# Optimization experiments

Hardware: AMD Instinct MI355X
Metric: run time of the kernel (lower is better)

Reference implementation:

```python
import jax, jax.numpy as jnp
import numpy as np

N = 100000
IN_DIM = 128
HID = 128
HEADS = 2
OUT_DIM = 2
E = 800000
NEG_SLOPE = 0.2


def setup_inputs() -> dict:
    key = jax.random.key(0)
    ks = jax.random.split(key, 12)
    x = jax.random.normal(ks[0], (N, IN_DIM), dtype=jnp.float32)
    edge_index = jax.random.randint(ks[1], (2, E), 0, N, dtype=jnp.int64)
    s = 0.05
    # GATConv layer 1: in=128 -> heads=2, out=128
    W1 = jax.random.normal(ks[2], (IN_DIM, HEADS * HID), dtype=jnp.float32) * s
    a_src1 = jax.random.normal(ks[3], (HEADS, HID), dtype=jnp.float32) * s
    a_dst1 = jax.random.normal(ks[4], (HEADS, HID), dtype=jnp.float32) * s
    b1 = jnp.zeros((HEADS * HID,), dtype=jnp.float32)
    # GATConv layer 2: in=256 -> heads=2, out=128
    W2 = jax.random.normal(ks[5], (HEADS * HID, HEADS * HID), dtype=jnp.float32) * s
    a_src2 = jax.random.normal(ks[6], (HEADS, HID), dtype=jnp.float32) * s
    a_dst2 = jax.random.normal(ks[7], (HEADS, HID), dtype=jnp.float32) * s
    b2 = jnp.zeros((HEADS * HID,), dtype=jnp.float32)
    # post_mp: Linear(256,128) -> Dropout(eval, no-op) -> Linear(128,2)
    Wp1 = jax.random.normal(ks[8], (HEADS * HID, HID), dtype=jnp.float32) * s
    bp1 = jnp.zeros((HID,), dtype=jnp.float32)
    Wp2 = jax.random.normal(ks[9], (HID, OUT_DIM), dtype=jnp.float32) * s
    bp2 = jnp.zeros((OUT_DIM,), dtype=jnp.float32)
    return {"x": x, "edge_index": edge_index,
            "W1": W1, "a_src1": a_src1, "a_dst1": a_dst1, "b1": b1,
            "W2": W2, "a_src2": a_src2, "a_dst2": a_dst2, "b2": b2,
            "Wp1": Wp1, "bp1": bp1, "Wp2": Wp2, "bp2": bp2}


def gat_conv(x, src, dst, W, a_src, a_dst, b):
    # linear transform, split heads: [N, H, C]
    h = (x @ W).reshape(-1, HEADS, HID)
    # per-node attention logits: [N, H]
    alpha_src = jnp.sum(h * a_src, axis=-1)
    alpha_dst = jnp.sum(h * a_dst, axis=-1)
    # per-edge logits, edge e = (src -> dst): [E, H]
    e = jax.nn.leaky_relu(alpha_src[src] + alpha_dst[dst], NEG_SLOPE)
    # segment softmax over incoming edges of each destination node
    m = jax.ops.segment_max(e, dst, num_segments=N)
    e = jnp.exp(e - m[dst])
    denom = jax.ops.segment_sum(e, dst, num_segments=N)
    alpha = e / (denom[dst] + 1e-16)
    # gather source features, weight, scatter-add to destinations
    msg = h[src] * alpha[:, :, None]            # [E, H, C]
    out = jax.ops.segment_sum(msg, dst, num_segments=N)  # [N, H, C]
    return out.reshape(-1, HEADS * HID) + b


def reference(x, edge_index, W1, a_src1, a_dst1, b1, W2, a_src2, a_dst2, b2,
              Wp1, bp1, Wp2, bp2):
    # add self-loops (PyG GATConv default)
    loops = jnp.arange(N, dtype=edge_index.dtype)
    src = jnp.concatenate([edge_index[0], loops])
    dst = jnp.concatenate([edge_index[1], loops])
    h = jax.nn.relu(gat_conv(x, src, dst, W1, a_src1, a_dst1, b1))
    h = jax.nn.relu(gat_conv(h, src, dst, W2, a_src2, a_dst2, b2))
    h = h @ Wp1 + bp1          # post_mp Linear 1 (dropout is eval no-op)
    h = h @ Wp2 + bp2          # post_mp Linear 2
    return jax.nn.sigmoid(h)
```

## Files before the change

### kernel.cpp

```cpp
#include <hip/hip_runtime.h>
#include <hip/hip_bf16.h>
#include <math.h>

#define NNODES 100000
#define NPAD   100032
#define IN_DIM 128
#define HID 128
#define HEADS 2
#define F2 256
#define NEDGES 800000
#define ETOT 900000
#define NEG_SLOPE 0.2f
#define MB 1563
#define EDGE_BLOCKS 3516

typedef unsigned int uint;
typedef unsigned short ushort;
typedef __attribute__((ext_vector_type(8))) short short8;
typedef __attribute__((ext_vector_type(4))) float floatx4;

__device__ __forceinline__ ushort f2bf(float f) {
    uint u = __builtin_bit_cast(uint, f);
    u += 0x7fffu + ((u >> 16) & 1u);
    return (ushort)(u >> 16);
}
__device__ __forceinline__ float bf2f(uint u16) {
    return __builtin_bit_cast(float, u16 << 16);
}
__device__ __forceinline__ float wred_sum(float v) {
    for (int o = 32; o; o >>= 1) v += __shfl_xor(v, o);
    return v;
}

__device__ __forceinline__ void gld16(const ushort* g, ushort* l) {
    __builtin_amdgcn_global_load_lds(
        (const __attribute__((address_space(1))) unsigned int*)(uintptr_t)g,
        (__attribute__((address_space(3))) unsigned int*)(unsigned int)(uintptr_t)l,
        16, 0, 0);
}

__global__ __launch_bounds__(256) void scan1_kernel(const int* __restrict__ deg,
                                                    int* __restrict__ row_start,
                                                    int* __restrict__ bsum) {
    __shared__ int s[256];
    int t = threadIdx.x;
    int i = blockIdx.x * 256 + t;
    int v = (i < NNODES) ? deg[i] : 0;
    s[t] = v;
    __syncthreads();
    for (int off = 1; off < 256; off <<= 1) {
        int x = (t >= off) ? s[t - off] : 0;
        __syncthreads();
        s[t] += x;
        __syncthreads();
    }
    if (i < NNODES) row_start[i] = s[t] - v;
    if (t == 255) bsum[blockIdx.x] = s[255];
}

__global__ __launch_bounds__(256) void scan_fix_kernel(int* __restrict__ row_start,
                                                       const int* __restrict__ bsum,
                                                       int* __restrict__ cursor) {
    __shared__ int sh[256];
    int t = threadIdx.x, bid = blockIdx.x;
    int v = 0;
    for (int k = t; k < bid; k += 256) v += bsum[k];
    sh[t] = v;
    __syncthreads();
    for (int off = 128; off; off >>= 1) {
        if (t < off) sh[t] += sh[t + off];
        __syncthreads();
    }
    int boff = sh[0];
    int i = bid * 256 + t;
    if (i == 0) row_start[NNODES] = ETOT;
    if (i < NNODES) {
        int r = row_start[i] + boff;
        row_start[i] = r;
        cursor[i] = r;
    }
}

__global__ __launch_bounds__(256) void prep_hist_kernel(const int* __restrict__ ei,
                                                        int* __restrict__ deg,
                                                        const float* __restrict__ W1,
                                                        ushort* __restrict__ W1t,
                                                        const float* __restrict__ W2,
                                                        ushort* __restrict__ W2t,
                                                        const float* __restrict__ Wp1,
                                                        const float* __restrict__ bp1,
                                                        const float* __restrict__ Wp2,
                                                        const float* __restrict__ bp2,
                                                        float2* __restrict__ Wf,
                                                        float* __restrict__ bfv,
                                                        const float* __restrict__ x,
                                                        ushort* __restrict__ xbf) {
    int b = blockIdx.x, t = threadIdx.x;
    if (b < EDGE_BLOCKS) {
        int i = b * 256 + t;
        if (i < ETOT) {
            int dst = (i < NEDGES) ? ei[NEDGES + i] : (i - NEDGES);
            atomicAdd(&deg[dst], 1);
        }
        return;
    }
    int bb = b - EDGE_BLOCKS;
    if (bb < 128) {
        int i = bb * 256 + t;
        int n = i >> 7, k = i & 127;
        W1t[n * 128 + k] = f2bf(W1[k * 256 + n]);
    } else if (bb < 384) {
        int i = (bb - 128) * 256 + t;
        int n = i >> 8, k = i & 255;
        W2t[n * 256 + k] = f2bf(W2[k * 256 + n]);
    } else if (bb == 384) {
        float s0 = 0.f, s1 = 0.f;
        for (int m = 0; m < 128; m++) {
            float w = Wp1[t * 128 + m];
            s0 += w * Wp2[2 * m];
            s1 += w * Wp2[2 * m + 1];
        }
        Wf[t] = make_float2(s0, s1);
        if (t < 2) {
            float bb2 = bp2[t];
            for (int m = 0; m < 128; m++) bb2 += bp1[m] * Wp2[2 * m + t];
            bfv[t] = bb2;
        }
    } else {
        size_t i = (size_t)(bb - 385) * 2048 + t * 8;
        float4 f0 = *reinterpret_cast<const float4*>(&x[i]);
        float4 f1 = *reinterpret_cast<const float4*>(&x[i + 4]);
        uint4 o;
        o.x = (uint)f2bf(f0.x) | ((uint)f2bf(f0.y) << 16);
        o.y = (uint)f2bf(f0.z) | ((uint)f2bf(f0.w) << 16);
        o.z = (uint)f2bf(f1.x) | ((uint)f2bf(f1.y) << 16);
        o.w = (uint)f2bf(f1.z) | ((uint)f2bf(f1.w) << 16);
        *reinterpret_cast<uint4*>(&xbf[i]) = o;
    }
}

__device__ __forceinline__ void gemm_body(int mb, int head,
                                          const ushort* __restrict__ A,
                                          const ushort* __restrict__ Bt,
                                          ushort* __restrict__ C,
                                          float* __restrict__ as_f,
                                          float* __restrict__ ad_f,
                                          const float* __restrict__ aS,
                                          const float* __restrict__ aD,
                                          int K, ushort* smem) {
    int t = threadIdx.x;
    int wave = t >> 6, lane = t & 63;
    int quad = lane >> 4, l16 = lane & 15;
    size_t rowBase = (size_t)mb * 64;
    int colBase = head * 128;

    floatx4 acc[8];
#pragma unroll
    for (int i = 0; i < 8; i++) acc[i] = (floatx4){0.f, 0.f, 0.f, 0.f};

    int srow = lane >> 2;
    int scg  = (lane & 3) ^ ((lane >> 3) & 3);
    const ushort* gA  = A  + (rowBase + wave * 16 + srow) * (size_t)K + scg * 8;
    const ushort* gB0 = Bt + (size_t)(colBase + wave * 16 + srow) * K + scg * 8;
    const ushort* gB1 = gB0 + (size_t)64 * K;
    ushort* lA  = smem + wave * 512;
    ushort* lB0 = smem + 2048 + wave * 512;
    ushort* lB1 = lB0 + 2048;

    const char* sb = (const char*)smem;
    int xs = (quad ^ ((l16 >> 1) & 3)) * 16;
    int aoff = (wave * 16 + l16) * 64 + xs;
    int boff = 4096 + l16 * 64 + xs;

    for (int k0 = 0; k0 < K; k0 += 32) {
        gld16(gA + k0, lA);
        gld16(gB0 + k0, lB0);
        gld16(gB1 + k0, lB1);
        __syncthreads();
        union { uint4 u; short8 s; } afr, bfr;
        afr.u = *reinterpret_cast<const uint4*>(sb + aoff);
#pragma unroll
        for (int nt = 0; nt < 8; nt++) {
            bfr.u = *reinterpret_cast<const uint4*>(sb + boff + nt * 1024);
            acc[nt] = __builtin_amdgcn_mfma_f32_16x16x32_bf16(afr.s, bfr.s, acc[nt], 0, 0, 0);
        }
        __syncthreads();
    }

    {
        float aSv[8], aDv[8];
#pragma unroll
        for (int nt = 0; nt < 8; nt++) {
            int c = colBase + nt * 16 + l16;
            aSv[nt] = aS[c];
            aDv[nt] = aD[c];
        }
#pragma unroll
        for (int r = 0; r < 4; r++) {
            float ps = 0.f, pd = 0.f;
#pragma unroll
            for (int nt = 0; nt < 8; nt++) {
                ps += acc[nt][r] * aSv[nt];
                pd += acc[nt][r] * aDv[nt];
            }
#pragma unroll
            for (int o = 1; o < 16; o <<= 1) {
                ps += __shfl_xor(ps, o);
                pd += __shfl_xor(pd, o);
            }
            if (l16 == 0) {
                size_t row = rowBase + wave * 16 + quad * 4 + r;
                as_f[2 * row + head] = ps;
                ad_f[2 * row + head] = pd;
            }
        }
    }

    ushort* lbuf = smem;
#pragma unroll
    for (int half = 0; half < 2; half++) {
        __syncthreads();
#pragma unroll
        for (int nt4 = 0; nt4 < 4; nt4++) {
            int nt = half * 4 + nt4;
            int col = nt4 * 16 + l16;
#pragma unroll
            for (int r = 0; r < 4; r++) {
                int row = wave * 16 + quad * 4 + r;
                lbuf[row * 72 + col] = f2bf(acc[nt][r]);
            }
        }
        __syncthreads();
        int row = t >> 2;
        int ch = t & 3;
        uint4 v0 = *reinterpret_cast<const uint4*>(&lbuf[row * 72 + ch * 8]);
        uint4 v1 = *reinterpret_cast<const uint4*>(&lbuf[row * 72 + 32 + ch * 8]);
        size_t g = (rowBase + row) * (size_t)F2 + colBase + half * 64;
        *reinterpret_cast<uint4*>(&C[g + ch * 8]) = v0;
        *reinterpret_cast<uint4*>(&C[g + 32 + ch * 8]) = v1;
    }
}

__global__ __launch_bounds__(256) void scatter_gemm_kernel(const int* __restrict__ ei,
                                                           int* __restrict__ cursor,
                                                           int* __restrict__ csr_src,
                                                           const ushort* __restrict__ A,
                                                           const ushort* __restrict__ Bt,
                                                           ushort* __restrict__ C,
                                                           float* __restrict__ as_f,
                                                           float* __restrict__ ad_f,
                                                           const float* __restrict__ aS,
                                                           const float* __restrict__ aD,
                                                           int K) {
    __shared__ ushort smem[6144];
    int b = blockIdx.x;
    if (b < EDGE_BLOCKS) {
        int i = b * 256 + threadIdx.x;
        if (i < ETOT) {
            int src, dst;
            if (i < NEDGES) { src = ei[i]; dst = ei[NEDGES + i]; }
            else            { src = i - NEDGES; dst = src; }
            int pos = atomicAdd(&cursor[dst], 1);
            csr_src[pos] = src;
        }
        return;
    }
    int gb = b - EDGE_BLOCKS;
    int head = gb >= MB;
    int mb = head ? gb - MB : gb;
    gemm_body(mb, head, A, Bt, C, as_f, ad_f, aS, aD, K, smem);
}

__global__ __launch_bounds__(256) void mfma_gemm(const ushort* __restrict__ A,
                                                 const ushort* __restrict__ Bt,
                                                 ushort* __restrict__ C,
                                                 float* __restrict__ as_f,
                                                 float* __restrict__ ad_f,
                                                 const float* __restrict__ aS,
                                                 const float* __restrict__ aD,
                                                 int K) {
    __shared__ ushort smem[6144];
    gemm_body(blockIdx.x, blockIdx.y, A, Bt, C, as_f, ad_f, aS, aD, K, smem);
}

__device__ __forceinline__ float edge_w(float2 q, float adsel, bool head1) {
    float l = (head1 ? q.y : q.x) + adsel;
    l = l > 0.f ? l : NEG_SLOPE * l;
    return __expf(l);
}

__global__ __launch_bounds__(256) void gather_kernel(const uint2* __restrict__ hb2,
                                                     const int* __restrict__ row_start,
                                                     const int* __restrict__ csr_src,
                                                     const float2* __restrict__ as_,
                                                     const float2* __restrict__ ad_,
                                                     const float4* __restrict__ bias4,
                                                     uint2* __restrict__ outb2,
                                                     const float4* __restrict__ WfA,
                                                     const float* __restrict__ bfv,
                                                     float2* __restrict__ outp,
                                                     int final_mode,
                                                     int nbase, int nlimit) {
    int wave = threadIdx.x >> 6, lane = threadIdx.x & 63;
    int n = nbase + blockIdx.x * 4 + wave;
    if (n >= nlimit) return;
    int beg = row_start[n], end = row_start[n + 1];
    float2 ad = ad_[n];
    bool head1 = lane >= 32;
    float adsel = head1 ? ad.y : ad.x;

    float a0 = 0.f, a1 = 0.f, a2 = 0.f, a3 = 0.f;
    float aden = 0.f;

    int j = beg;
    for (; j + 3 < end; j += 4) {
        int s0 = csr_src[j],     s1 = csr_src[j + 1];
        int s2 = csr_src[j + 2], s3 = csr_src[j + 3];
        float2 q0 = as_[s0], q1 = as_[s1], q2 = as_[s2], q3 = as_[s3];
        uint2 h0 = hb2[(size_t)s0 * 64 + lane];
        uint2 h1 = hb2[(size_t)s1 * 64 + lane];
        uint2 h2 = hb2[(size_t)s2 * 64 + lane];
        uint2 h3 = hb2[(size_t)s3 * 64 + lane];
        float w0 = edge_w(q0, adsel, head1), w1 = edge_w(q1, adsel, head1);
        float w2 = edge_w(q2, adsel, head1), w3 = edge_w(q3, adsel, head1);
        aden += (w0 + w1) + (w2 + w3);
        a0 += w0 * bf2f(h0.x & 0xffffu) + w1 * bf2f(h1.x & 0xffffu)
            + w2 * bf2f(h2.x & 0xffffu) + w3 * bf2f(h3.x & 0xffffu);
        a1 += w0 * bf2f(h0.x >> 16) + w1 * bf2f(h1.x >> 16)
            + w2 * bf2f(h2.x >> 16) + w3 * bf2f(h3.x >> 16);
        a2 += w0 * bf2f(h0.y & 0xffffu) + w1 * bf2f(h1.y & 0xffffu)
            + w2 * bf2f(h2.y & 0xffffu) + w3 * bf2f(h3.y & 0xffffu);
        a3 += w0 * bf2f(h0.y >> 16) + w1 * bf2f(h1.y >> 16)
            + w2 * bf2f(h2.y >> 16) + w3 * bf2f(h3.y >> 16);
    }
    for (; j < end; j++) {
        int s = csr_src[j];
        float2 q = as_[s];
        uint2 hv = hb2[(size_t)s * 64 + lane];
        float w = edge_w(q, adsel, head1);
        aden += w;
        a0 += w * bf2f(hv.x & 0xffffu);
        a1 += w * bf2f(hv.x >> 16);
        a2 += w * bf2f(hv.y & 0xffffu);
        a3 += w * bf2f(hv.y >> 16);
    }

    float inv = 1.f / (aden + 1e-16f);
    float4 b = bias4[lane];
    float o0 = fmaxf(a0 * inv + b.x, 0.f);
    float o1 = fmaxf(a1 * inv + b.y, 0.f);
    float o2 = fmaxf(a2 * inv + b.z, 0.f);
    float o3 = fmaxf(a3 * inv + b.w, 0.f);
    if (!final_mode) {
        uint2 pk;
        pk.x = (uint)f2bf(o0) | ((uint)f2bf(o1) << 16);
        pk.y = (uint)f2bf(o2) | ((uint)f2bf(o3) << 16);
        outb2[(size_t)n * 64 + lane] = pk;
    } else {
        float4 wa = WfA[2 * lane];
        float4 wb = WfA[2 * lane + 1];
        float p0 = o0 * wa.x + o1 * wa.z + o2 * wb.x + o3 * wb.z;
        float p1 = o0 * wa.y + o1 * wa.w + o2 * wb.y + o3 * wb.w;
        p0 = wred_sum(p0);
        p1 = wred_sum(p1);
        if (lane == 0) {
            float2 r;
            r.x = 1.f / (1.f + __expf(-(p0 + bfv[0])));
            r.y = 1.f / (1.f + __expf(-(p1 + bfv[1])));
            outp[n] = r;
        }
    }
}

extern "C" void kernel_launch(void* const* d_in, const int* in_sizes, int n_in,
                              void* d_out, int out_size, void* d_ws, size_t ws_size,
                              hipStream_t stream) {
    const float* x      = (const float*)d_in[0];
    const int*   ei     = (const int*)d_in[1];
    const float* W1     = (const float*)d_in[2];
    const float* a_src1 = (const float*)d_in[3];
    const float* a_dst1 = (const float*)d_in[4];
    const float* b1     = (const float*)d_in[5];
    const float* W2     = (const float*)d_in[6];
    const float* a_src2 = (const float*)d_in[7];
    const float* a_dst2 = (const float*)d_in[8];
    const float* b2     = (const float*)d_in[9];
    const float* Wp1    = (const float*)d_in[10];
    const float* bp1    = (const float*)d_in[11];
    const float* Wp2    = (const float*)d_in[12];
    const float* bp2    = (const float*)d_in[13];
    float* outp = (float*)d_out;

    char* w = (char*)d_ws;
    ushort* xbf  = (ushort*)w; w += (size_t)NPAD * 128 * sizeof(ushort);
    ushort* hbf  = (ushort*)w; w += (size_t)NPAD * 256 * sizeof(ushort);
    ushort* obf  = (ushort*)w; w += (size_t)NPAD * 256 * sizeof(ushort);
    ushort* W1t  = (ushort*)w; w += (size_t)256 * 128 * sizeof(ushort);
    ushort* W2t  = (ushort*)w; w += (size_t)256 * 256 * sizeof(ushort);
    float2* Wf   = (float2*)w; w += 256 * sizeof(float2);
    float*  bfv  = (float*)w;  w += 4 * sizeof(float);
    float2* as_  = (float2*)w; w += (size_t)NPAD * sizeof(float2);
    float2* ad_  = (float2*)w; w += (size_t)NPAD * sizeof(float2);
    int* deg       = (int*)w; w += (size_t)NNODES * sizeof(int);
    int* row_start = (int*)w; w += (size_t)(NNODES + 16) * sizeof(int);
    int* cursor    = (int*)w; w += (size_t)NNODES * sizeof(int);
    int* csr_src   = (int*)w; w += (size_t)ETOT * sizeof(int);
    int* bsum      = (int*)w; w += 512 * sizeof(int);

    const int SCAN_BLOCKS = (NNODES + 255) / 256;
    const int HALF_BLOCKS = 12500;

    hipMemsetAsync(deg, 0, (size_t)NNODES * sizeof(int), stream);

    prep_hist_kernel<<<EDGE_BLOCKS + 6635, 256, 0, stream>>>(
        ei, deg, W1, W1t, W2, W2t, Wp1, bp1, Wp2, bp2, Wf, bfv, x, xbf);

    scan1_kernel<<<SCAN_BLOCKS, 256, 0, stream>>>(deg, row_start, bsum);
    scan_fix_kernel<<<SCAN_BLOCKS, 256, 0, stream>>>(row_start, bsum, cursor);

    scatter_gemm_kernel<<<EDGE_BLOCKS + 2 * MB, 256, 0, stream>>>(
        ei, cursor, csr_src, xbf, W1t, hbf, (float*)as_, (float*)ad_,
        a_src1, a_dst1, 128);

    gather_kernel<<<HALF_BLOCKS, 256, 0, stream>>>((const uint2*)hbf, row_start, csr_src,
                                                   as_, ad_, (const float4*)b1, (uint2*)obf,
                                                   (const float4*)Wf, bfv, (float2*)outp,
                                                   0, 0, 50000);
    gather_kernel<<<HALF_BLOCKS, 256, 0, stream>>>((const uint2*)hbf, row_start, csr_src,
                                                   as_, ad_, (const float4*)b1, (uint2*)obf,
                                                   (const float4*)Wf, bfv, (float2*)outp,
                                                   0, 50000, NNODES);

    mfma_gemm<<<dim3(MB, 2), 256, 0, stream>>>(obf, W2t, hbf, (float*)as_, (float*)ad_,
                                               a_src2, a_dst2, 256);
    gather_kernel<<<HALF_BLOCKS, 256, 0, stream>>>((const uint2*)hbf, row_start, csr_src,
                                                   as_, ad_, (const float4*)b2, (uint2*)obf,
                                                   (const float4*)Wf, bfv, (float2*)outp,
                                                   1, 0, 50000);
    gather_kernel<<<HALF_BLOCKS, 256, 0, stream>>>((const uint2*)hbf, row_start, csr_src,
                                                   as_, ad_, (const float4*)b2, (uint2*)obf,
                                                   (const float4*)Wf, bfv, (float2*)outp,
                                                   1, 50000, NNODES);
}
```

Measured before the change: 448.3 us.

## Load GEMM fragments directly from global memory with 128-row tiles

The GEMM body no longer stages A and B through LDS with global_load_lds and barriers. Each wave now loads its MFMA fragments straight from global memory and computes two 16-row subtiles, so a block covers 128 rows instead of 64. K becomes a template parameter so the loops can be unrolled. This removes the per-k-step __syncthreads and halves the number of GEMM blocks, at the cost of more registers, redundant global B loads across waves (reliant on L2/L1 hits), and uncoalesced 16-byte row-strided loads.

```diff
diff --git a/kernel.cpp b/kernel.cpp
--- a/kernel.cpp
+++ b/kernel.cpp
@@ -3,7 +3,7 @@
 #include <math.h>
 
 #define NNODES 100000
-#define NPAD   100032
+#define NPAD   100096
 #define IN_DIM 128
 #define HID 128
 #define HEADS 2
@@ -11,7 +11,7 @@
 #define NEDGES 800000
 #define ETOT 900000
 #define NEG_SLOPE 0.2f
-#define MB 1563
+#define MB2 782
 #define EDGE_BLOCKS 3516
 
 typedef unsigned int uint;
@@ -30,13 +30,6 @@
 __device__ __forceinline__ float wred_sum(float v) {
     for (int o = 32; o; o >>= 1) v += __shfl_xor(v, o);
     return v;
-}
-
-__device__ __forceinline__ void gld16(const ushort* g, ushort* l) {
-    __builtin_amdgcn_global_load_lds(
-        (const __attribute__((address_space(1))) unsigned int*)(uintptr_t)g,
-        (__attribute__((address_space(3))) unsigned int*)(unsigned int)(uintptr_t)l,
-        16, 0, 0);
 }
 
 __global__ __launch_bounds__(256) void scan1_kernel(const int* __restrict__ deg,
@@ -139,6 +132,7 @@
     }
 }
 
+template<int K>
 __device__ __forceinline__ void gemm_body(int mb, int head,
                                           const ushort* __restrict__ A,
                                           const ushort* __restrict__ Bt,
@@ -147,44 +141,38 @@
                                           float* __restrict__ ad_f,
                                           const float* __restrict__ aS,
                                           const float* __restrict__ aD,
-                                          int K, ushort* smem) {
+                                          ushort* smem) {
     int t = threadIdx.x;
     int wave = t >> 6, lane = t & 63;
     int quad = lane >> 4, l16 = lane & 15;
-    size_t rowBase = (size_t)mb * 64;
+    size_t rowBase = (size_t)mb * 128;
     int colBase = head * 128;
 
-    floatx4 acc[8];
-#pragma unroll
-    for (int i = 0; i < 8; i++) acc[i] = (floatx4){0.f, 0.f, 0.f, 0.f};
-
-    int srow = lane >> 2;
-    int scg  = (lane & 3) ^ ((lane >> 3) & 3);
-    const ushort* gA  = A  + (rowBase + wave * 16 + srow) * (size_t)K + scg * 8;
-    const ushort* gB0 = Bt + (size_t)(colBase + wave * 16 + srow) * K + scg * 8;
-    const ushort* gB1 = gB0 + (size_t)64 * K;
-    ushort* lA  = smem + wave * 512;
-    ushort* lB0 = smem + 2048 + wave * 512;
-    ushort* lB1 = lB0 + 2048;
-
-    const char* sb = (const char*)smem;
-    int xs = (quad ^ ((l16 >> 1) & 3)) * 16;
-    int aoff = (wave * 16 + l16) * 64 + xs;
-    int boff = 4096 + l16 * 64 + xs;
+    floatx4 acc[2][8];
+#pragma unroll
+    for (int s = 0; s < 2; s++)
+#pragma unroll
+        for (int i = 0; i < 8; i++) acc[s][i] = (floatx4){0.f, 0.f, 0.f, 0.f};
+
+    const ushort* gA0 = A + (rowBase + wave * 32 + l16) * (size_t)K + quad * 8;
+    const ushort* gA1 = gA0 + (size_t)16 * K;
+    const ushort* gB[8];
+#pragma unroll
+    for (int nt = 0; nt < 8; nt++)
+        gB[nt] = Bt + (size_t)(colBase + nt * 16 + l16) * K + quad * 8;
 
     for (int k0 = 0; k0 < K; k0 += 32) {
-        gld16(gA + k0, lA);
-        gld16(gB0 + k0, lB0);
-        gld16(gB1 + k0, lB1);
-        __syncthreads();
-        union { uint4 u; short8 s; } afr, bfr;
-        afr.u = *reinterpret_cast<const uint4*>(sb + aoff);
+        union { uint4 u; short8 s; } a0, a1, bf[8];
+        a0.u = *reinterpret_cast<const uint4*>(gA0 + k0);
+        a1.u = *reinterpret_cast<const uint4*>(gA1 + k0);
+#pragma unroll
+        for (int nt = 0; nt < 8; nt++)
+            bf[nt].u = *reinterpret_cast<const uint4*>(gB[nt] + k0);
 #pragma unroll
         for (int nt = 0; nt < 8; nt++) {
-            bfr.u = *reinterpret_cast<const uint4*>(sb + boff + nt * 1024);
-            acc[nt] = __builtin_amdgcn_mfma_f32_16x16x32_bf16(afr.s, bfr.s, acc[nt], 0, 0, 0);
-        }
-        __syncthreads();
+            acc[0][nt] = __builtin_amdgcn_mfma_f32_16x16x32_bf16(a0.s, bf[nt].s, acc[0][nt], 0, 0, 0);
+            acc[1][nt] = __builtin_amdgcn_mfma_f32_16x16x32_bf16(a1.s, bf[nt].s, acc[1][nt], 0, 0, 0);
+        }
     }
 
     {
@@ -196,27 +184,29 @@
             aDv[nt] = aD[c];
         }
 #pragma unroll
-        for (int r = 0; r < 4; r++) {
-            float ps = 0.f, pd = 0.f;
-#pragma unroll
-            for (int nt = 0; nt < 8; nt++) {
-                ps += acc[nt][r] * aSv[nt];
-                pd += acc[nt][r] * aDv[nt];
+        for (int s = 0; s < 2; s++) {
+#pragma unroll
+            for (int r = 0; r < 4; r++) {
+                float ps = 0.f, pd = 0.f;
+#pragma unroll
+                for (int nt = 0; nt < 8; nt++) {
+                    ps += acc[s][nt][r] * aSv[nt];
+                    pd += acc[s][nt][r] * aDv[nt];
+                }
+#pragma unroll
+                for (int o = 1; o < 16; o <<= 1) {
+                    ps += __shfl_xor(ps, o);
+                    pd += __shfl_xor(pd, o);
+                }
+                if (l16 == 0) {
+                    size_t row = rowBase + wave * 32 + s * 16 + quad * 4 + r;
+                    as_f[2 * row + head] = ps;
+                    ad_f[2 * row + head] = pd;
+                }
             }
-#pragma unroll
-            for (int o = 1; o < 16; o <<= 1) {
-                ps += __shfl_xor(ps, o);
-                pd += __shfl_xor(pd, o);
-            }
-            if (l16 == 0) {
-                size_t row = rowBase + wave * 16 + quad * 4 + r;
-                as_f[2 * row + head] = ps;
-                ad_f[2 * row + head] = pd;
-            }
-        }
-    }
-
-    ushort* lbuf = smem;
+        }
+    }
+
 #pragma unroll
     for (int half = 0; half < 2; half++) {
         __syncthreads();
@@ -225,19 +215,21 @@
             int nt = half * 4 + nt4;
             int col = nt4 * 16 + l16;
 #pragma unroll
-            for (int r = 0; r < 4; r++) {
-                int row = wave * 16 + quad * 4 + r;
-                lbuf[row * 72 + col] = f2bf(acc[nt][r]);
-            }
+            for (int s = 0; s < 2; s++)
+#pragma unroll
+                for (int r = 0; r < 4; r++) {
+                    int row = wave * 32 + s * 16 + quad * 4 + r;
+                    smem[row * 72 + col] = f2bf(acc[s][nt][r]);
+                }
         }
         __syncthreads();
-        int row = t >> 2;
-        int ch = t & 3;
-        uint4 v0 = *reinterpret_cast<const uint4*>(&lbuf[row * 72 + ch * 8]);
-        uint4 v1 = *reinterpret_cast<const uint4*>(&lbuf[row * 72 + 32 + ch * 8]);
-        size_t g = (rowBase + row) * (size_t)F2 + colBase + half * 64;
-        *reinterpret_cast<uint4*>(&C[g + ch * 8]) = v0;
-        *reinterpret_cast<uint4*>(&C[g + 32 + ch * 8]) = v1;
+        int row = t >> 1;
+        int co = (t & 1) * 32;
+        const uint4* src = reinterpret_cast<const uint4*>(&smem[row * 72 + co]);
+        uint4 v0 = src[0], v1 = src[1], v2 = src[2], v3 = src[3];
+        uint4* dst = reinterpret_cast<uint4*>(
+            &C[(rowBase + row) * (size_t)F2 + colBase + half * 64 + co]);
+        dst[0] = v0; dst[1] = v1; dst[2] = v2; dst[3] = v3;
     }
 }
 
@@ -250,9 +242,8 @@
                                                            float* __restrict__ as_f,
                                                            float* __restrict__ ad_f,
                                                            const float* __restrict__ aS,
-                                                           const float* __restrict__ aD,
-                                                           int K) {
-    __shared__ ushort smem[6144];
+                                                           const float* __restrict__ aD) {
+    __shared__ ushort smem[9216];
     int b = blockIdx.x;
     if (b < EDGE_BLOCKS) {
         int i = b * 256 + threadIdx.x;
@@ -266,21 +257,20 @@
         return;
     }
     int gb = b - EDGE_BLOCKS;
-    int head = gb >= MB;
-    int mb = head ? gb - MB : gb;
-    gemm_body(mb, head, A, Bt, C, as_f, ad_f, aS, aD, K, smem);
-}
-
-__global__ __launch_bounds__(256) void mfma_gemm(const ushort* __restrict__ A,
-                                                 const ushort* __restrict__ Bt,
-                                                 ushort* __restrict__ C,
-                                                 float* __restrict__ as_f,
-                                                 float* __restrict__ ad_f,
-                                                 const float* __restrict__ aS,
-                                                 const float* __restrict__ aD,
-                                                 int K) {
-    __shared__ ushort smem[6144];
-    gemm_body(blockIdx.x, blockIdx.y, A, Bt, C, as_f, ad_f, aS, aD, K, smem);
+    int head = gb >= MB2;
+    int mb = head ? gb - MB2 : gb;
+    gemm_body<128>(mb, head, A, Bt, C, as_f, ad_f, aS, aD, smem);
+}
+
+__global__ __launch_bounds__(256) void mfma_gemm_k256(const ushort* __restrict__ A,
+                                                      const ushort* __restrict__ Bt,
+                                                      ushort* __restrict__ C,
+                                                      float* __restrict__ as_f,
+                                                      float* __restrict__ ad_f,
+                                                      const float* __restrict__ aS,
+                                                      const float* __restrict__ aD) {
+    __shared__ ushort smem[9216];
+    gemm_body<256>(blockIdx.x, blockIdx.y, A, Bt, C, as_f, ad_f, aS, aD, smem);
 }
 
 __device__ __forceinline__ float edge_w(float2 q, float adsel, bool head1) {
@@ -418,9 +408,9 @@
     scan1_kernel<<<SCAN_BLOCKS, 256, 0, stream>>>(deg, row_start, bsum);
     scan_fix_kernel<<<SCAN_BLOCKS, 256, 0, stream>>>(row_start, bsum, cursor);
 
-    scatter_gemm_kernel<<<EDGE_BLOCKS + 2 * MB, 256, 0, stream>>>(
+    scatter_gemm_kernel<<<EDGE_BLOCKS + 2 * MB2, 256, 0, stream>>>(
         ei, cursor, csr_src, xbf, W1t, hbf, (float*)as_, (float*)ad_,
-        a_src1, a_dst1, 128);
+        a_src1, a_dst1);
 
     gather_kernel<<<HALF_BLOCKS, 256, 0, stream>>>((const uint2*)hbf, row_start, csr_src,
                                                    as_, ad_, (const float4*)b1, (uint2*)obf,
@@ -431,8 +421,8 @@
                                                    (const float4*)Wf, bfv, (float2*)outp,
                                                    0, 50000, NNODES);
 
-    mfma_gemm<<<dim3(MB, 2), 256, 0, stream>>>(obf, W2t, hbf, (float*)as_, (float*)ad_,
-                                               a_src2, a_dst2, 256);
+    mfma_gemm_k256<<<dim3(MB2, 2), 256, 0, stream>>>(obf, W2t, hbf, (float*)as_, (float*)ad_,
+                                                     a_src2, a_dst2);
     gather_kernel<<<HALF_BLOCKS, 256, 0, stream>>>((const uint2*)hbf, row_start, csr_src,
                                                    as_, ad_, (const float4*)b2, (uint2*)obf,
                                                    (const float4*)Wf, bfv, (float2*)outp,
```

After: 523.1 us. 1.17x slower.
